# Optimization experiments

Measured on AMD Instinct MI355X. Metric: run time of the kernel, lower is better.

The kernel has to match this reference:

```python
import math
import jax, jax.numpy as jnp
import numpy as np


def _alibi_slopes(n_heads: int) -> np.ndarray:
    def pow2_slopes(n):
        start = 2 ** (-2 ** (-(math.log2(n) - 3)))
        return [start * (start ** i) for i in range(n)]
    if n_heads & (n_heads - 1) == 0:
        slopes = pow2_slopes(n_heads)
    else:
        closest = 2 ** math.floor(math.log2(n_heads))
        slopes = pow2_slopes(closest)
        extra_base = 2 ** (-2 ** (-(math.log2(2 * closest) - 3)))
        slopes.extend(extra_base * (extra_base ** i) for i in range(n_heads - closest))
        slopes = slopes[:n_heads]
    return np.asarray(slopes, dtype=np.float32)


def setup_inputs() -> dict:
    B, T, C, H = 2, 2048, 768, 12
    key = jax.random.key(0)
    ks = jax.random.split(key, 6)
    return {
        "x_norm_for_qk": jax.random.normal(ks[0], (B, T, C), jnp.float32),
        "xt_current_for_v": jax.random.normal(ks[1], (B, T, C), jnp.float32),
        "W_attn": jax.random.normal(ks[2], (2 * C, C), jnp.float32) * 0.02,  # nn.Linear weight [out,in]
        "b_attn": jnp.zeros((2 * C,), jnp.float32),
        "v_tmp": jax.random.normal(ks[3], (H, H), jnp.float32) * 0.02,
        "proj_tmp": jax.random.normal(ks[4], (H, H), jnp.float32) * 0.02,
    }


def reference(x_norm_for_qk, xt_current_for_v, W_attn, b_attn, v_tmp, proj_tmp):
    B, T, C = x_norm_for_qk.shape
    H = v_tmp.shape[0]
    hd = C // H

    # Q,K projection: Linear(C -> 2C), then split.
    qk = x_norm_for_qk @ W_attn.T + b_attn  # [B,T,2C]
    q, k = jnp.split(qk, 2, axis=-1)
    q = q.reshape(B, T, H, hd).transpose(0, 2, 1, 3)  # [B,H,T,hd]
    k = k.reshape(B, T, H, hd).transpose(0, 2, 1, 3)

    # Kronecker-lifted V: block (i,j) of the CxC matrix is v_tmp[i,j]*I(hd),
    # so applying it mixes only across heads per head-dim channel.
    xt = xt_current_for_v.reshape(B, T, H, hd)
    v = jnp.einsum("ij,btjd->btid", v_tmp, xt).transpose(0, 2, 1, 3)  # [B,H,T,hd]

    scale = 1.0 / math.sqrt(hd)
    scores = jnp.einsum("bhqd,bhkd->bhqk", q, k) * scale  # [B,H,T,T]

    # ALiBi bias with causal mask (-inf above diagonal).
    slopes = jnp.asarray(_alibi_slopes(H))  # [H]
    pos = jnp.arange(T, dtype=jnp.float32)
    rel = pos[None, :] - pos[:, None]  # [T,T], memory - context
    causal = pos[None, :] <= pos[:, None]
    bias = jnp.where(causal[None], slopes[:, None, None] * rel[None], -jnp.inf)  # [H,T,T]
    scores = scores + bias[None]

    att = jax.nn.softmax(scores, axis=-1)  # dropout p=0 -> identity
    y = jnp.einsum("bhqk,bhkd->bhqd", att, v)  # [B,H,T,hd]
    y = y.transpose(0, 2, 1, 3)  # [B,T,H,hd]

    # Kronecker-lifted output projection.
    y = jnp.einsum("ij,btjd->btid", proj_tmp, y)
    return y.reshape(B, T, C)
```

## Files before the change

kernel.cpp:

```cpp
#include <hip/hip_runtime.h>
#include <hip/hip_bf16.h>
#include <math.h>

#define TSEQ 2048
#define CDIM 768
#define NH   12
#define HD   64

typedef __attribute__((ext_vector_type(8))) short bf16x8;
typedef __attribute__((ext_vector_type(4))) float f32x4;

union Bf8 { bf16x8 v; __hip_bfloat16 e[8]; };

__constant__ float c_slopes2[12] = {
    0.72134752f, 0.36067376f, 0.18033688f, 0.09016844f,
    0.04508422f, 0.02254211f, 0.011271055f, 0.0056355275f,
    1.02015692f, 0.72134752f, 0.51007846f, 0.36067376f
};
#define M2 4.3280851f
#define QSCALE 0.18033688f
#define EXP2F(x) __builtin_amdgcn_exp2f(x)

__device__ __forceinline__ unsigned pack2(float lo, float hi) {
    union { __hip_bfloat162 b; unsigned u; } cv;
    cv.b = __float22bfloat162_rn(make_float2(lo, hi));
    return cv.u;
}
__device__ __forceinline__ unsigned short bf16bits(float x) {
    union { __hip_bfloat16 b; unsigned short s; } cv;
    cv.b = __float2bfloat16(x);
    return cv.s;
}

#define MFMA16(a, b, c) __builtin_amdgcn_mfma_f32_16x16x32_bf16(a, b, c, 0, 0, 0)

__global__ __launch_bounds__(512) void gemm_qk(
    const float* __restrict__ X,
    const float* __restrict__ W,
    const float* __restrict__ bias,
    __hip_bfloat16* __restrict__ Qb,
    __hip_bfloat16* __restrict__ Kt)
{
    __shared__ alignas(16) __hip_bfloat16 As[128][40];
    __shared__ alignas(16) __hip_bfloat16 Bs[128][40];

    const int tid  = threadIdx.x;
    const int lane = tid & 63;
    const int w    = tid >> 6;
    const int lg   = lane >> 4;
    const int lc   = lane & 15;
    const int m0   = blockIdx.y * 128;
    const int n0   = blockIdx.x * 128;
    const int m0w  = (w >> 2) * 64;
    const int n0w  = (w & 3) * 32;

    const int srow = tid >> 2;
    const int scol = (tid & 3) * 8;

    f32x4 acc[4][2] = {};

    for (int k0 = 0; k0 < CDIM; k0 += 32) {
        __syncthreads();
        {
            const float* xp = X + (size_t)(m0 + srow) * CDIM + k0 + scol;
            const float* wp = W + (size_t)(n0 + srow) * CDIM + k0 + scol;
            float4 a0 = *(const float4*)(xp);
            float4 a1 = *(const float4*)(xp + 4);
            float4 b0 = *(const float4*)(wp);
            float4 b1 = *(const float4*)(wp + 4);
            Bf8 av, bv;
            av.e[0]=__float2bfloat16(a0.x); av.e[1]=__float2bfloat16(a0.y);
            av.e[2]=__float2bfloat16(a0.z); av.e[3]=__float2bfloat16(a0.w);
            av.e[4]=__float2bfloat16(a1.x); av.e[5]=__float2bfloat16(a1.y);
            av.e[6]=__float2bfloat16(a1.z); av.e[7]=__float2bfloat16(a1.w);
            bv.e[0]=__float2bfloat16(b0.x); bv.e[1]=__float2bfloat16(b0.y);
            bv.e[2]=__float2bfloat16(b0.z); bv.e[3]=__float2bfloat16(b0.w);
            bv.e[4]=__float2bfloat16(b1.x); bv.e[5]=__float2bfloat16(b1.y);
            bv.e[6]=__float2bfloat16(b1.z); bv.e[7]=__float2bfloat16(b1.w);
            *(bf16x8*)&As[srow][scol] = av.v;
            *(bf16x8*)&Bs[srow][scol] = bv.v;
        }
        __syncthreads();

        bf16x8 af[4], bfr[2];
        #pragma unroll
        for (int mt = 0; mt < 4; ++mt)
            af[mt] = *(const bf16x8*)&As[m0w + mt*16 + lc][lg*8];
        #pragma unroll
        for (int nt = 0; nt < 2; ++nt)
            bfr[nt] = *(const bf16x8*)&Bs[n0w + nt*16 + lc][lg*8];
        #pragma unroll
        for (int mt = 0; mt < 4; ++mt)
            #pragma unroll
            for (int nt = 0; nt < 2; ++nt)
                acc[mt][nt] = MFMA16(af[mt], bfr[nt], acc[mt][nt]);
    }

    #pragma unroll
    for (int mt = 0; mt < 4; ++mt) {
        #pragma unroll
        for (int nt = 0; nt < 2; ++nt) {
            int n  = n0 + n0w + nt*16 + lc;
            float bv = bias[n];
            #pragma unroll
            for (int r = 0; r < 4; ++r) {
                int m = m0 + m0w + mt*16 + lg*4 + r;
                float v = acc[mt][nt][r] + bv;
                int b = m >> 11, t = m & (TSEQ-1);
                if (n < CDIM) {
                    int h = n >> 6, dd = n & 63;
                    Qb[(((size_t)(b*NH + h))*TSEQ + t)*HD + dd] = __float2bfloat16(v * QSCALE);
                } else {
                    int n2 = n - CDIM;
                    int h = n2 >> 6, dd = n2 & 63;
                    int bh_ = b*NH + h;
                    int kb = t >> 5, tt = t & 31;
                    int j  = ((tt >> 4) << 1) + (dd >> 5);
                    int ln = (((dd >> 3) & 3) << 4) + (tt & 15);
                    Kt[((size_t)(bh_*64 + kb))*2048 + j*512 + ln*8 + (dd & 7)] =
                        __float2bfloat16(v);
                }
            }
        }
    }
}

__global__ __launch_bounds__(256) void vmix(
    const float* __restrict__ XT, const float* __restrict__ vtmp,
    __hip_bfloat16* __restrict__ Vb)
{
    __shared__ float vm[144];
    if (threadIdx.x < 144) vm[threadIdx.x] = vtmp[threadIdx.x];
    __syncthreads();
    int idx = blockIdx.x * 256 + threadIdx.x;
    int dd = idx & 63;
    int bt = idx >> 6;
    int t = bt & (TSEQ-1), b = bt >> 11;
    float xv[12];
    #pragma unroll
    for (int j = 0; j < 12; ++j) xv[j] = XT[(size_t)bt*CDIM + j*64 + dd];
    #pragma unroll
    for (int i = 0; i < 12; ++i) {
        float s = 0.f;
        #pragma unroll
        for (int j = 0; j < 12; ++j) s += vm[i*12+j] * xv[j];
        Vb[(((size_t)(b*NH + i))*TSEQ + t)*HD + dd] = __float2bfloat16(s);
    }
}

__global__ __launch_bounds__(256) void vtrans(
    const __hip_bfloat16* __restrict__ Vb, __hip_bfloat16* __restrict__ Vt)
{
    __shared__ __hip_bfloat16 Ls[64][65];
    const int bh = blockIdx.y;
    const int t0 = blockIdx.x * 64;
    const int tid = threadIdx.x;
    const int r8 = tid >> 3;
    const int c8 = (tid & 7) * 8;

    #pragma unroll
    for (int it = 0; it < 2; ++it) {
        int t = it*32 + r8;
        Bf8 v; v.v = *(const bf16x8*)(Vb + ((size_t)bh*TSEQ + t0 + t)*HD + c8);
        #pragma unroll
        for (int j = 0; j < 8; ++j) Ls[t][c8 + j] = v.e[j];
    }
    __syncthreads();
    #pragma unroll
    for (int it = 0; it < 2; ++it) {
        int d = it*32 + r8;
        Bf8 v;
        #pragma unroll
        for (int j = 0; j < 8; ++j) v.e[j] = Ls[c8 + j][d];
        int kb = (t0 + c8) >> 5;
        int ko = (t0 + c8) & 31;
        *(bf16x8*)(Vt + (size_t)bh*(HD*TSEQ) + kb*2048 + d*32 + ko) = v.v;
    }
}

__global__ __launch_bounds__(256, 3) void attn8(
    const __hip_bfloat16* __restrict__ Qb,
    const __hip_bfloat16* __restrict__ Kt,
    const __hip_bfloat16* __restrict__ Vt,
    __hip_bfloat16* __restrict__ Y)
{
    __shared__ float Osh[4][2][64][20];
    __shared__ float Lsh[4][2][16];

    const int tid  = threadIdx.x;
    const int lane = tid & 63;
    const int w    = tid >> 6;
    const int lg   = lane >> 4;
    const int lc   = lane & 15;

    const int id  = blockIdx.x;
    const int id2 = (id & 7) * 96 + (id >> 3);
    const int bx  = id2 & 31;
    const int bh  = id2 >> 5;

    const float slope = c_slopes2[bh % NH];
    const __hip_bfloat16* Qp = Qb + (size_t)bh * TSEQ * HD;
    const __hip_bfloat16* Kp = Kt + (size_t)bh * 64 * 2048;
    const __hip_bfloat16* Vp = Vt + (size_t)bh * (HD * TSEQ);

    const float slgl  = slope * (float)(lg * 4);
    const float slp16 = slope * 16.0f;
    const int   s01   = lc + ((lg & 1) << 5);
    const int   s23   = s01 + 16;
    const bool  hiK   = (lg >= 2);

    bf16x8 kA0, kA1, kA2, kA3, kB0, kB1, kB2, kB3;

#define LOADK(S, TI) do {                                                       \
    const __hip_bfloat16* kp_ = Kp + (size_t)(TI)*2048 + lane*8;                \
    k##S##0 = *(const bf16x8*)(kp_);                                            \
    k##S##1 = *(const bf16x8*)(kp_ + 512);                                      \
    k##S##2 = *(const bf16x8*)(kp_ + 1024);                                     \
    k##S##3 = *(const bf16x8*)(kp_ + 1536);                                     \
} while (0);

#define SHUF(P_, x0, x1, x2, x3)                                                \
    {                                                                           \
        int t00 = __shfl((int)x0, s01), t02 = __shfl((int)x2, s01);             \
        int t10 = __shfl((int)x1, s01), t12 = __shfl((int)x3, s01);             \
        int t20 = __shfl((int)x0, s23), t22 = __shfl((int)x2, s23);             \
        int t30 = __shfl((int)x1, s23), t32 = __shfl((int)x3, s23);             \
        P_.u[0] = hiK ? (unsigned)t02 : (unsigned)t00;                          \
        P_.u[1] = hiK ? (unsigned)t12 : (unsigned)t10;                          \
        P_.u[2] = hiK ? (unsigned)t22 : (unsigned)t20;                          \
        P_.u[3] = hiK ? (unsigned)t32 : (unsigned)t30;                          \
    }

#define CONS(TI, S) do {                                                        \
    const int K0C = (TI) * 32;                                                  \
    const __hip_bfloat16* vb_ = Vp + (size_t)(TI)*2048 + lc*32 + lg*8;          \
    bf16x8 v0_ = *(const bf16x8*)(vb_);                                         \
    bf16x8 v1_ = *(const bf16x8*)(vb_ + 512);                                   \
    bf16x8 v2_ = *(const bf16x8*)(vb_ + 1024);                                  \
    bf16x8 v3_ = *(const bf16x8*)(vb_ + 1536);                                  \
    f32x4 s0a = {}, s0b = {}, s1a = {}, s1b = {};                               \
    s0a = MFMA16(k##S##0, qfa0, s0a); s0a = MFMA16(k##S##1, qfa1, s0a);         \
    s0b = MFMA16(k##S##0, qfb0, s0b); s0b = MFMA16(k##S##1, qfb1, s0b);         \
    s1a = MFMA16(k##S##2, qfa0, s1a); s1a = MFMA16(k##S##3, qfa1, s1a);         \
    s1b = MFMA16(k##S##2, qfb0, s1b); s1b = MFMA16(k##S##3, qfb1, s1b);         \
    float base0_ = fmaf((float)K0C, slope, slgl);                               \
    float pa0[4], pa1[4], pb0[4], pb1[4];                                       \
    _Pragma("unroll")                                                           \
    for (int r = 0; r < 4; ++r) {                                               \
        float bk_  = base0_ + slope * (float)r;                                 \
        float bk1_ = bk_ + slp16;                                               \
        int kk0_ = K0C + lg*4 + r, kk1_ = kk0_ + 16;                            \
        float e0a = EXP2F(s0a[r] + (bk_  - eqa));                               \
        float e1a = EXP2F(s1a[r] + (bk1_ - eqa));                               \
        float e0b = EXP2F(s0b[r] + (bk_  - eqb));                               \
        float e1b = EXP2F(s1b[r] + (bk1_ - eqb));                               \
        pa0[r] = (kk0_ <= qia) ? e0a : 0.f;                                     \
        pa1[r] = (kk1_ <= qia) ? e1a : 0.f;                                     \
        pb0[r] = (kk0_ <= qib) ? e0b : 0.f;                                     \
        pb1[r] = (kk1_ <= qib) ? e1b : 0.f;                                     \
        lsa += pa0[r] + pa1[r];                                                 \
        lsb += pb0[r] + pb1[r];                                                 \
    }                                                                           \
    unsigned a0_ = pack2(pa0[0], pa0[1]), a1_ = pack2(pa0[2], pa0[3]);          \
    unsigned a2_ = pack2(pa1[0], pa1[1]), a3_ = pack2(pa1[2], pa1[3]);          \
    unsigned b0_ = pack2(pb0[0], pb0[1]), b1_ = pack2(pb0[2], pb0[3]);          \
    unsigned b2_ = pack2(pb1[0], pb1[1]), b3_ = pack2(pb1[2], pb1[3]);          \
    union { unsigned u[4]; bf16x8 v; } PA_, PB_;                                \
    SHUF(PA_, a0_, a1_, a2_, a3_)                                               \
    SHUF(PB_, b0_, b1_, b2_, b3_)                                               \
    Oa[0] = MFMA16(v0_, PA_.v, Oa[0]); Ob[0] = MFMA16(v0_, PB_.v, Ob[0]);       \
    Oa[1] = MFMA16(v1_, PA_.v, Oa[1]); Ob[1] = MFMA16(v1_, PB_.v, Ob[1]);       \
    Oa[2] = MFMA16(v2_, PA_.v, Oa[2]); Ob[2] = MFMA16(v2_, PB_.v, Ob[2]);       \
    Oa[3] = MFMA16(v3_, PA_.v, Oa[3]); Ob[3] = MFMA16(v3_, PB_.v, Ob[3]);       \
} while (0);

    auto runMember = [&](int qb, bool first) {
        const int q0m = qb * 32;
        const int qia = q0m + lc;
        const int qib = q0m + 16 + lc;
        const float eqa = slope * (float)qia + M2;
        const float eqb = slope * (float)qib + M2;

        bf16x8 qfa0 = *(const bf16x8*)(Qp + (size_t)qia * HD + lg*8);
        bf16x8 qfa1 = *(const bf16x8*)(Qp + (size_t)qia * HD + 32 + lg*8);
        bf16x8 qfb0 = *(const bf16x8*)(Qp + (size_t)qib * HD + lg*8);
        bf16x8 qfb1 = *(const bf16x8*)(Qp + (size_t)qib * HD + 32 + lg*8);

        f32x4 Oa[4] = {}; f32x4 Ob[4] = {};
        float lsa = 0.f, lsb = 0.f;

        const int myN = (qb >= w) ? ((qb - w) >> 2) + 1 : 0;

        if (myN > 0) {
            LOADK(A, w)
            int j = 0;
            while (true) {
                if (j + 1 < myN) LOADK(B, w + 4*(j+1))
                CONS(w + 4*j, A)
                ++j; if (j >= myN) break;
                if (j + 1 < myN) LOADK(A, w + 4*(j+1))
                CONS(w + 4*j, B)
                ++j; if (j >= myN) break;
            }
        }

        lsa += __shfl_xor(lsa, 16); lsa += __shfl_xor(lsa, 32);
        lsb += __shfl_xor(lsb, 16); lsb += __shfl_xor(lsb, 32);

        if (!first) __syncthreads();
        #pragma unroll
        for (int dt = 0; dt < 4; ++dt) {
            *(f32x4*)&Osh[w][0][lane][dt*4] = Oa[dt];
            *(f32x4*)&Osh[w][1][lane][dt*4] = Ob[dt];
        }
        if (lane < 16) {
            Lsh[w][0][lane] = lsa;
            Lsh[w][1][lane] = lsb;
        }
        __syncthreads();

        #pragma unroll
        for (int h = 0; h < 2; ++h) {
            f32x4 o = (h == 0) ? Oa[w] : Ob[w];
            #pragma unroll
            for (int w2 = 0; w2 < 4; ++w2)
                if (w2 != w) o += *(const f32x4*)&Osh[w2][h][lane][w*4];
            float lt = Lsh[0][h][lc] + Lsh[1][h][lc] + Lsh[2][h][lc] + Lsh[3][h][lc];
            float inv = 1.0f / lt;
            int q = q0m + h*16 + lc;
            ushort4 u;
            u.x = bf16bits(o[0] * inv);
            u.y = bf16bits(o[1] * inv);
            u.z = bf16bits(o[2] * inv);
            u.w = bf16bits(o[3] * inv);
            *(ushort4*)(Y + ((size_t)bh*TSEQ + q)*HD + w*16 + lg*4) = u;
        }
    };

    runMember(bx, true);
    runMember(63 - bx, false);

#undef LOADK
#undef SHUF
#undef CONS
}

__global__ __launch_bounds__(256) void projmix(
    const __hip_bfloat16* __restrict__ Y, const float* __restrict__ ptmp,
    float* __restrict__ Out)
{
    __shared__ float pm[144];
    if (threadIdx.x < 144) pm[threadIdx.x] = ptmp[threadIdx.x];
    __syncthreads();
    int idx = blockIdx.x * 256 + threadIdx.x;
    int dd = idx & 63;
    int bt = idx >> 6;
    int t = bt & (TSEQ-1), b = bt >> 11;
    float yv[12];
    #pragma unroll
    for (int j = 0; j < 12; ++j)
        yv[j] = __bfloat162float(Y[(((size_t)(b*NH + j))*TSEQ + t)*HD + dd]);
    #pragma unroll
    for (int i = 0; i < 12; ++i) {
        float s = 0.f;
        #pragma unroll
        for (int j = 0; j < 12; ++j) s += pm[i*12+j] * yv[j];
        Out[(size_t)bt*CDIM + i*64 + dd] = s;
    }
}

extern "C" void kernel_launch(void* const* d_in, const int* in_sizes, int n_in,
                              void* d_out, int out_size, void* d_ws, size_t ws_size,
                              hipStream_t stream) {
    (void)in_sizes; (void)n_in; (void)out_size; (void)ws_size;
    const float* X    = (const float*)d_in[0];
    const float* XT   = (const float*)d_in[1];
    const float* W    = (const float*)d_in[2];
    const float* bias = (const float*)d_in[3];
    const float* vtmp = (const float*)d_in[4];
    const float* ptmp = (const float*)d_in[5];
    float* Out = (float*)d_out;

    char* ws = (char*)d_ws;
    const size_t BHTD = (size_t)2 * NH * TSEQ * HD;
    __hip_bfloat16* Qb = (__hip_bfloat16*)ws;
    __hip_bfloat16* Kt = (__hip_bfloat16*)(ws + BHTD*2);
    __hip_bfloat16* Vb = (__hip_bfloat16*)(ws + BHTD*4);
    __hip_bfloat16* Vt = (__hip_bfloat16*)(ws + BHTD*6);
    __hip_bfloat16* Yb = (__hip_bfloat16*)(ws + BHTD*8);

    gemm_qk<<<dim3(12, 32), 512, 0, stream>>>(X, W, bias, Qb, Kt);
    vmix<<<1024, 256, 0, stream>>>(XT, vtmp, Vb);
    vtrans<<<dim3(32, 24), 256, 0, stream>>>(Vb, Vt);
    attn8<<<768, 256, 0, stream>>>(Qb, Kt, Vt, Yb);
    projmix<<<1024, 256, 0, stream>>>(Yb, ptmp, Out);
}
```

Baseline: 84.57 us.

## Split attention key range across eight waves per block instead of four

```diff
diff --git a/kernel.cpp b/kernel.cpp
--- a/kernel.cpp
+++ b/kernel.cpp
@@ -178,14 +178,14 @@
     }
 }
 
-__global__ __launch_bounds__(256, 3) void attn8(
+__global__ __launch_bounds__(512, 6) void attn9(
     const __hip_bfloat16* __restrict__ Qb,
     const __hip_bfloat16* __restrict__ Kt,
     const __hip_bfloat16* __restrict__ Vt,
     __hip_bfloat16* __restrict__ Y)
 {
-    __shared__ float Osh[4][2][64][20];
-    __shared__ float Lsh[4][2][16];
+    __shared__ float Osh[8][64][20];
+    __shared__ float Lsh[8][16];
 
     const int tid  = threadIdx.x;
     const int lane = tid & 63;
@@ -289,17 +289,17 @@
         f32x4 Oa[4] = {}; f32x4 Ob[4] = {};
         float lsa = 0.f, lsb = 0.f;
 
-        const int myN = (qb >= w) ? ((qb - w) >> 2) + 1 : 0;
+        const int myN = (qb >= w) ? ((qb - w) >> 3) + 1 : 0;
 
         if (myN > 0) {
             LOADK(A, w)
             int j = 0;
             while (true) {
-                if (j + 1 < myN) LOADK(B, w + 4*(j+1))
-                CONS(w + 4*j, A)
+                if (j + 1 < myN) LOADK(B, w + 8*(j+1))
+                CONS(w + 8*j, A)
                 ++j; if (j >= myN) break;
-                if (j + 1 < myN) LOADK(A, w + 4*(j+1))
-                CONS(w + 4*j, B)
+                if (j + 1 < myN) LOADK(A, w + 8*(j+1))
+                CONS(w + 8*j, B)
                 ++j; if (j >= myN) break;
             }
         }
@@ -309,31 +309,51 @@
 
         if (!first) __syncthreads();
         #pragma unroll
-        for (int dt = 0; dt < 4; ++dt) {
-            *(f32x4*)&Osh[w][0][lane][dt*4] = Oa[dt];
-            *(f32x4*)&Osh[w][1][lane][dt*4] = Ob[dt];
-        }
-        if (lane < 16) {
-            Lsh[w][0][lane] = lsa;
-            Lsh[w][1][lane] = lsb;
-        }
+        for (int dt = 0; dt < 4; ++dt)
+            *(f32x4*)&Osh[w][lane][dt*4] = Oa[dt];
+        if (lane < 16) Lsh[w][lane] = lsa;
         __syncthreads();
-
-        #pragma unroll
-        for (int h = 0; h < 2; ++h) {
-            f32x4 o = (h == 0) ? Oa[w] : Ob[w];
-            #pragma unroll
-            for (int w2 = 0; w2 < 4; ++w2)
-                if (w2 != w) o += *(const f32x4*)&Osh[w2][h][lane][w*4];
-            float lt = Lsh[0][h][lc] + Lsh[1][h][lc] + Lsh[2][h][lc] + Lsh[3][h][lc];
+        if (w < 4) {
+            f32x4 o = {};
+            #pragma unroll
+            for (int w2 = 0; w2 < 8; ++w2)
+                o += *(const f32x4*)&Osh[w2][lane][w*4];
+            float lt = 0.f;
+            #pragma unroll
+            for (int w2 = 0; w2 < 8; ++w2) lt += Lsh[w2][lc];
             float inv = 1.0f / lt;
-            int q = q0m + h*16 + lc;
+            int q = q0m + lc;
             ushort4 u;
             u.x = bf16bits(o[0] * inv);
             u.y = bf16bits(o[1] * inv);
             u.z = bf16bits(o[2] * inv);
             u.w = bf16bits(o[3] * inv);
             *(ushort4*)(Y + ((size_t)bh*TSEQ + q)*HD + w*16 + lg*4) = u;
+        }
+
+        __syncthreads();
+        #pragma unroll
+        for (int dt = 0; dt < 4; ++dt)
+            *(f32x4*)&Osh[w][lane][dt*4] = Ob[dt];
+        if (lane < 16) Lsh[w][lane] = lsb;
+        __syncthreads();
+        if (w >= 4) {
+            const int s = w & 3;
+            f32x4 o = {};
+            #pragma unroll
+            for (int w2 = 0; w2 < 8; ++w2)
+                o += *(const f32x4*)&Osh[w2][lane][s*4];
+            float lt = 0.f;
+            #pragma unroll
+            for (int w2 = 0; w2 < 8; ++w2) lt += Lsh[w2][lc];
+            float inv = 1.0f / lt;
+            int q = q0m + 16 + lc;
+            ushort4 u;
+            u.x = bf16bits(o[0] * inv);
+            u.y = bf16bits(o[1] * inv);
+            u.z = bf16bits(o[2] * inv);
+            u.w = bf16bits(o[3] * inv);
+            *(ushort4*)(Y + ((size_t)bh*TSEQ + q)*HD + s*16 + lg*4) = u;
         }
     };
 
@@ -392,6 +412,6 @@
     gemm_qk<<<dim3(12, 32), 512, 0, stream>>>(X, W, bias, Qb, Kt);
     vmix<<<1024, 256, 0, stream>>>(XT, vtmp, Vb);
     vtrans<<<dim3(32, 24), 256, 0, stream>>>(Vb, Vt);
-    attn8<<<768, 256, 0, stream>>>(Qb, Kt, Vt, Yb);
+    attn9<<<768, 512, 0, stream>>>(Qb, Kt, Vt, Yb);
     projmix<<<1024, 256, 0, stream>>>(Yb, ptmp, Out);
 }
```

Result: slower. 284.2 us (+236.0%).
